# Kernel tuning notes

Hardware: AMD Instinct MI355X
Metric: run time of the kernel (lower is better)

Reference implementation:

```python
import jax, jax.numpy as jnp
import numpy as np

NUM_SPECIAL = 3  # rows 1..NUM_SPECIAL in special table; row 0 is padding (zeros)

def setup_inputs() -> dict:
    key = jax.random.key(0)
    ks = jax.random.split(key, 16)
    T, B, E, H, L, V = 128, 32, 512, 512, 2, 32000
    G = 4 * H
    s = 0.02
    special_emb = jax.random.normal(ks[1], (NUM_SPECIAL + 1, E), jnp.float32) * s
    special_emb = special_emb.at[0].set(0.0)  # padding_idx=0
    return {
        "ids": jax.random.randint(ks[0], (T, B), 0, V),
        "length_countdown": jax.random.uniform(ks[2], (T, B, 1), jnp.float32),
        "word_emb": jax.random.normal(ks[3], (V, E), jnp.float32) * s,
        "special_emb": special_emb,
        "h0": jax.random.normal(ks[4], (L, B, H), jnp.float32) * s,
        "c0": jax.random.normal(ks[5], (L, B, H), jnp.float32) * s,
        "prev_output": jnp.zeros((B, H), jnp.float32),
        "Wih0": jax.random.normal(ks[6], (G, E + H + 1), jnp.float32) * s,
        "Whh0": jax.random.normal(ks[7], (G, H), jnp.float32) * s,
        "bih0": jnp.zeros((G,), jnp.float32),
        "bhh0": jnp.zeros((G,), jnp.float32),
        "Wih1": jax.random.normal(ks[8], (G, H), jnp.float32) * s,
        "Whh1": jax.random.normal(ks[9], (G, H), jnp.float32) * s,
        "bih1": jnp.zeros((G,), jnp.float32),
        "bhh1": jnp.zeros((G,), jnp.float32),
        "Wg": jax.random.normal(ks[10], (V, H), jnp.float32) * s,
        "bg": jnp.zeros((V,), jnp.float32),
    }

def _lstm_cell(x, h, c, Wih, Whh, bih, bhh):
    gates = x @ Wih.T + bih + h @ Whh.T + bhh  # [B, 4H]
    i, f, g, o = jnp.split(gates, 4, axis=-1)  # torch LSTMCell gate order
    c_new = jax.nn.sigmoid(f) * c + jax.nn.sigmoid(i) * jnp.tanh(g)
    h_new = jax.nn.sigmoid(o) * jnp.tanh(c_new)
    return h_new, c_new

def reference(ids, length_countdown, word_emb, special_emb, h0, c0, prev_output,
              Wih0, Whh0, bih0, bhh0, Wih1, Whh1, bih1, bhh1, Wg, bg):
    # embeddings = word_embeddings(ids) + special_embeddings(special_ids(ids))
    sp_ids = jnp.where(ids < NUM_SPECIAL, ids + 1, 0)
    emb = word_emb[ids] + special_emb[sp_ids]                 # [T,B,E]
    rnn_in = jnp.concatenate([emb, length_countdown], axis=2)  # [T,B,E+1]

    Wihs = (Wih0, Wih1); Whhs = (Whh0, Whh1)
    bihs = (bih0, bih1); bhhs = (bhh0, bhh1)
    L = h0.shape[0]

    def step(carry, emb_t):
        out, h, c = carry
        x = jnp.concatenate([emb_t, out], axis=1)  # input feeding
        hs, cs = [], []
        for l in range(L):
            h_l, c_l = _lstm_cell(x, h[l], c[l], Wihs[l], Whhs[l], bihs[l], bhhs[l])
            x = h_l  # dropout=0
            hs.append(h_l); cs.append(c_l)
        out = x
        score = jax.nn.log_softmax(out @ Wg.T + bg, axis=-1)  # generator
        return (out, jnp.stack(hs), jnp.stack(cs)), score

    (out, hT, cT), scores = jax.lax.scan(step, (prev_output, h0, c0), rnn_in)
    return scores, (hT, cT), out
```

## Files before the change

kernel.cpp:

```cpp
#include <hip/hip_runtime.h>
#include <hip/hip_bf16.h>


typedef __attribute__((ext_vector_type(8))) short bf16x8;
typedef __attribute__((ext_vector_type(4))) float f32x4;
typedef __attribute__((ext_vector_type(2))) unsigned long long u64x2;

#define AS1 __attribute__((address_space(1)))
#define AS3 __attribute__((address_space(3)))
#define RLX __ATOMIC_RELAXED
#define AGT __HIP_MEMORY_SCOPE_AGENT

__device__ __forceinline__ unsigned short f2bf(float f) {
  unsigned int u = __builtin_bit_cast(unsigned int, f);
  u += 0x7fffu + ((u >> 16) & 1u);
  return (unsigned short)(u >> 16);
}

__device__ __forceinline__ void gl16(const void* g, void* l) {
  __builtin_amdgcn_global_load_lds((const AS1 unsigned int*)g,
                                   (AS3 unsigned int*)l, 16, 0, 0);
}

__device__ __forceinline__ float sigm(float x) { return 1.0f / (1.0f + __expf(-x)); }

__global__ __launch_bounds__(256, 1) void prep_k(
    const float* __restrict__ Wg,  const float* __restrict__ Wih0,
    const float* __restrict__ Whh0,const float* __restrict__ Wih1,
    const float* __restrict__ Whh1,const float* __restrict__ bih0,
    const float* __restrict__ bhh0,const float* __restrict__ bih1,
    const float* __restrict__ bhh1,const float* __restrict__ h0,
    const float* __restrict__ pout,
    unsigned short* __restrict__ WgBf, unsigned short* __restrict__ W0e,
    unsigned short* __restrict__ Wr0p, unsigned short* __restrict__ Wr1p,
    float* __restrict__ b1p, float* __restrict__ bias0c,
    float* __restrict__ wcd, unsigned short* __restrict__ H0X,
    unsigned short* __restrict__ FOUT, unsigned short* __restrict__ H1I)
{
  const long N0 = 16384000L;
  const long N1 = N0 + 1048576L;
  const long N2 = N1 + 2097152L;
  const long N3 = N2 + 2097152L;
  const long N4 = N3 + 2048L;
  const long N5 = N4 + 2048L;
  const long N6 = N5 + 2048L;
  const long N7 = N6 + 49152L;
  for (long i = blockIdx.x * 256L + threadIdx.x; i < N7; i += 256L * gridDim.x) {
    if (i < N0) {
      WgBf[i] = f2bf(Wg[i]);
    } else if (i < N1) {
      long k = i - N0; int g = (int)(k >> 9); int kk = (int)(k & 511);
      W0e[k] = f2bf(Wih0[g * 1025 + kk]);
    } else if (i < N2) {
      long k = i - N1; int gp = (int)(k >> 10); int kk = (int)(k & 1023);
      int j = gp >> 2, gate = gp & 3; int g = gate * 512 + j;
      float v = (kk < 512) ? Whh0[g * 512 + kk] : Wih0[g * 1025 + 513 + (kk - 512)];
      Wr0p[k] = f2bf(v);
    } else if (i < N3) {
      long k = i - N2; int gp = (int)(k >> 10); int kk = (int)(k & 1023);
      int j = gp >> 2, gate = gp & 3; int g = gate * 512 + j;
      float v = (kk < 512) ? Wih1[g * 512 + kk] : Whh1[g * 512 + (kk - 512)];
      Wr1p[k] = f2bf(v);
    } else if (i < N4) {
      int gp = (int)(i - N3); int j = gp >> 2, gate = gp & 3; int g = gate * 512 + j;
      b1p[gp] = bih1[g] + bhh1[g];
    } else if (i < N5) {
      int g = (int)(i - N4); bias0c[g] = bih0[g] + bhh0[g];
    } else if (i < N6) {
      int g = (int)(i - N5); wcd[g] = Wih0[g * 1025 + 512];
    } else {
      long k = i - N6;
      int sub = (int)(k >> 14);
      int e = (int)(k & 16383);
      int wgx = e >> 9, b = (e >> 4) & 31, jl = e & 15;
      int j = wgx * 16 + jl;
      float v = (sub == 0) ? h0[b * 512 + j]
              : (sub == 1) ? h0[16384 + b * 512 + j]
                           : pout[b * 512 + j];
      unsigned short* dst = (sub == 0) ? H0X : (sub == 1) ? H1I : FOUT;
      dst[e] = f2bf(v);
    }
  }
}

__global__ __launch_bounds__(256, 1) void emb_k(
    const int* __restrict__ ids, const float* __restrict__ wemb,
    const float* __restrict__ semb, unsigned short* __restrict__ ebf)
{
  const int tb = blockIdx.x;
  const int id = ids[tb];
  const int sp = (id < 3) ? (id + 1) : 0;
  const float* wr = wemb + (long)id * 512;
  const float* sr = semb + sp * 512;
  for (int i = threadIdx.x; i < 512; i += 256)
    ebf[tb * 512 + i] = f2bf(wr[i] + sr[i]);
}

template<int EPI>
__global__ __launch_bounds__(256, 1) void gemm_bt(
    const unsigned short* __restrict__ A,
    const unsigned short* __restrict__ B, int N,
    float* __restrict__ C,
    const float* __restrict__ e0, float* __restrict__ e1,
    const float* __restrict__ e2)
{
  __shared__ unsigned short sA[4096];
  __shared__ unsigned short sB[4096];
  __shared__ float pmw[128][2][2];
  const int tid = threadIdx.x;
  const int l = tid & 63, w = tid >> 6;
  const int nb = N >> 7;
  const int bid = blockIdx.x;
  const int bm = bid / nb, bn = bid - bm * nb;

  const int u0 = w * 128 + l;
  const int u1 = u0 + 64;
  const int r0 = u0 >> 2, c0 = (u0 & 3) ^ (r0 & 3);
  const int r1 = u1 >> 2, c1 = (u1 & 3) ^ (r1 & 3);
  const unsigned short* ga0 = A + (long)(bm * 128 + r0) * 512 + c0 * 8;
  const unsigned short* ga1 = A + (long)(bm * 128 + r1) * 512 + c1 * 8;
  const unsigned short* gb0 = B + (long)(bn * 128 + r0) * 512 + c0 * 8;
  const unsigned short* gb1 = B + (long)(bn * 128 + r1) * 512 + c1 * 8;
  unsigned short* la0 = sA + (w * 2 + 0) * 512;
  unsigned short* la1 = sA + (w * 2 + 1) * 512;
  unsigned short* lb0 = sB + (w * 2 + 0) * 512;
  unsigned short* lb1 = sB + (w * 2 + 1) * 512;

  const int fr = l & 15, fc = l >> 4;
  const int wm = w >> 1, wn = w & 1;
  int aoff[4], boff[4];
#pragma unroll
  for (int mi = 0; mi < 4; ++mi) {
    int row = wm * 64 + mi * 16 + fr;
    aoff[mi] = row * 64 + ((fc ^ (row & 3)) * 16);
  }
#pragma unroll
  for (int ni = 0; ni < 4; ++ni) {
    int row = wn * 64 + ni * 16 + fr;
    boff[ni] = row * 64 + ((fc ^ (row & 3)) * 16);
  }

  f32x4 acc[4][4];
#pragma unroll
  for (int i = 0; i < 4; ++i)
#pragma unroll
    for (int jq = 0; jq < 4; ++jq) acc[i][jq] = (f32x4){0.f, 0.f, 0.f, 0.f};

  for (int kt = 0; kt < 16; ++kt) {
    __syncthreads();
    gl16(ga0 + kt * 32, la0);
    gl16(ga1 + kt * 32, la1);
    gl16(gb0 + kt * 32, lb0);
    gl16(gb1 + kt * 32, lb1);
    asm volatile("s_waitcnt vmcnt(0)" ::: "memory");
    __syncthreads();
    bf16x8 av[4], bv[4];
#pragma unroll
    for (int mi = 0; mi < 4; ++mi)
      av[mi] = *(const bf16x8*)((const char*)sA + aoff[mi]);
#pragma unroll
    for (int ni = 0; ni < 4; ++ni)
      bv[ni] = *(const bf16x8*)((const char*)sB + boff[ni]);
#pragma unroll
    for (int mi = 0; mi < 4; ++mi)
#pragma unroll
      for (int ni = 0; ni < 4; ++ni)
        acc[mi][ni] = __builtin_amdgcn_mfma_f32_16x16x32_bf16(av[mi], bv[ni], acc[mi][ni], 0, 0, 0);
  }

  const int mbase = bm * 128 + wm * 64;
  const int nbase = bn * 128 + wn * 64;

  if (EPI == 0) {
#pragma unroll
    for (int mi = 0; mi < 4; ++mi)
#pragma unroll
      for (int ni = 0; ni < 4; ++ni) {
        const int col = nbase + ni * 16 + fr;
#pragma unroll
        for (int r = 0; r < 4; ++r) {
          const int row = mbase + mi * 16 + fc * 4 + r;
          const int gp = ((row & 511) << 2) | (row >> 9);
          float v = acc[mi][ni][r] + e0[row] + e2[col] * e1[row];
          C[(long)gp * N + col] = v;
        }
      }
  } else {
    float m2[4][4], s2[4][4];
#pragma unroll
    for (int mi = 0; mi < 4; ++mi)
#pragma unroll
      for (int r = 0; r < 4; ++r) { m2[mi][r] = -3.0e38f; s2[mi][r] = 0.f; }
#pragma unroll
    for (int mi = 0; mi < 4; ++mi)
#pragma unroll
      for (int ni = 0; ni < 4; ++ni) {
        const int col = nbase + ni * 16 + fr;
        const float bgc = e0[col];
#pragma unroll
        for (int r = 0; r < 4; ++r) {
          float v = acc[mi][ni][r] + bgc;
          acc[mi][ni][r] = v;
          C[(long)(mbase + mi * 16 + fc * 4 + r) * N + col] = v;
          m2[mi][r] = fmaxf(m2[mi][r], v);
        }
      }
#pragma unroll
    for (int mi = 0; mi < 4; ++mi)
#pragma unroll
      for (int r = 0; r < 4; ++r)
#pragma unroll
        for (int s = 1; s < 16; s <<= 1)
          m2[mi][r] = fmaxf(m2[mi][r], __shfl_xor(m2[mi][r], s));
#pragma unroll
    for (int mi = 0; mi < 4; ++mi)
#pragma unroll
      for (int ni = 0; ni < 4; ++ni)
#pragma unroll
        for (int r = 0; r < 4; ++r)
          s2[mi][r] += __expf(acc[mi][ni][r] - m2[mi][r]);
#pragma unroll
    for (int mi = 0; mi < 4; ++mi)
#pragma unroll
      for (int r = 0; r < 4; ++r)
#pragma unroll
        for (int s = 1; s < 16; s <<= 1)
          s2[mi][r] += __shfl_xor(s2[mi][r], s);
    if (fr == 0) {
#pragma unroll
      for (int mi = 0; mi < 4; ++mi)
#pragma unroll
        for (int r = 0; r < 4; ++r) {
          const int rl = wm * 64 + mi * 16 + fc * 4 + r;
          pmw[rl][wn][0] = m2[mi][r];
          pmw[rl][wn][1] = s2[mi][r];
        }
    }
    __syncthreads();
    if (tid < 128) {
      float ma = pmw[tid][0][0], sa = pmw[tid][0][1];
      float mb = pmw[tid][1][0], sb = pmw[tid][1][1];
      float M = fmaxf(ma, mb);
      float S = sa * __expf(ma - M) + sb * __expf(mb - M);
      float2* PMS = (float2*)e1;
      float2 o; o.x = M; o.y = S;
      PMS[(long)(bm * 128 + tid) * nb + bn] = o;
    }
  }
}

__global__ __launch_bounds__(256, 1) void lstm_seq(
    const unsigned short* __restrict__ Wr0p,
    const unsigned short* __restrict__ Wr1p,
    const float* __restrict__ P0t, const float* __restrict__ b1p,
    const float* __restrict__ c0in,
    unsigned short* __restrict__ H0X, unsigned short* __restrict__ H1X,
    const unsigned short* __restrict__ FOUT, const unsigned short* __restrict__ H1I,
    unsigned short* __restrict__ outbf, float* __restrict__ outs,
    unsigned int* __restrict__ flagA, unsigned int* __restrict__ flagB)
{
  const int tid = threadIdx.x;
  const int wg = blockIdx.x;
  const int l = tid & 63, w = tid >> 6;
  const int fr = l & 15, fc = l >> 4;

  __shared__ unsigned short sx[32768];
  __shared__ float sg[32][65];
  __shared__ unsigned short sh[32][16];

  const int b = tid & 31, jl0 = tid >> 5;
  const int sb = l >> 1, sjh = l & 1;

  float c0r[2], c1r[2], h0k[2], h1k[2];
#pragma unroll
  for (int jq = 0; jq < 2; ++jq) {
    c0r[jq] = c0in[b * 512 + wg * 16 + jl0 + jq * 8];
    c1r[jq] = c0in[16384 + b * 512 + wg * 16 + jl0 + jq * 8];
    h0k[jq] = 0.f; h1k[jq] = 0.f;
  }

  float b1v[8];
#pragma unroll
  for (int jq = 0; jq < 2; ++jq)
#pragma unroll
    for (int g = 0; g < 4; ++g)
      b1v[jq * 4 + g] = b1p[(wg * 16 + jl0 + jq * 8) * 4 + g];

  const char* sxb0 = (const char*)sx + fr * 2048;
  const char* sxb1 = (const char*)sx + (16 + fr) * 2048;
  const int xr = (fr & 7) << 4;
  const int wrow = (wg * 64 + w * 16 + fr) * 1024 + fc * 8;

  char* const sxw = (char*)sx + sb * 2048;
  const int sswz = (sb & 7) << 4;

#define STAGE2(srcp, half)                                                    \
  do {                                                                        \
    unsigned long long q0[8], q1[8];                                          \
    _Pragma("unroll")                                                         \
    for (int i = 0; i < 8; ++i) {                                             \
      int u = i * 256 + tid;                                                  \
      q0[i] = __hip_atomic_load((const unsigned long long*)(srcp) + u * 2,    \
                                RLX, AGT);                                    \
      q1[i] = __hip_atomic_load((const unsigned long long*)(srcp) + u * 2 + 1,\
                                RLX, AGT);                                    \
    }                                                                         \
    _Pragma("unroll")                                                         \
    for (int i = 0; i < 8; ++i) {                                             \
      int cb = (half) * 1024 + (i * 4 + w) * 32 + sjh * 16;                   \
      u64x2 v; v.x = q0[i]; v.y = q1[i];                                      \
      *(u64x2*)(sxw + (cb ^ sswz)) = v;                                       \
    }                                                                         \
  } while (0)

#define MFMA_HALF(Wp, k0, a0v, a1v)                                           \
  do {                                                                        \
    _Pragma("unroll")                                                         \
    for (int kt = (k0); kt < (k0) + 16; ++kt) {                               \
      bf16x8 bv = *(const bf16x8*)((Wp) + wrow + kt * 32);                    \
      bf16x8 x0 = *(const bf16x8*)(sxb0 + ((kt * 64 + fc * 16) ^ xr));        \
      bf16x8 x1 = *(const bf16x8*)(sxb1 + ((kt * 64 + fc * 16) ^ xr));        \
      a0v = __builtin_amdgcn_mfma_f32_16x16x32_bf16(x0, bv, a0v, 0, 0, 0);    \
      a1v = __builtin_amdgcn_mfma_f32_16x16x32_bf16(x1, bv, a1v, 0, 0, 0);    \
    }                                                                         \
  } while (0)

#define POLL(flags, tgt)                                                      \
  do {                                                                        \
    const unsigned int* fp = (flags) + ((l & 31) << 5);                       \
    for (;;) {                                                                \
      unsigned int f = __hip_atomic_load(fp, RLX, AGT);                       \
      if (__all((int)(f >= (unsigned int)(tgt)))) break;                      \
      __builtin_amdgcn_s_sleep(1);                                            \
    }                                                                         \
    asm volatile("" ::: "memory");                                            \
  } while (0)

  STAGE2(H0X, 0);
  __syncthreads();
  if (tid == 0)
    __hip_atomic_store(&flagB[wg << 5], 1u, RLX, AGT);

  for (int t = 0; t < 128; ++t) {
    float p0v[8];
#pragma unroll
    for (int jq = 0; jq < 2; ++jq)
#pragma unroll
      for (int g = 0; g < 4; ++g)
        p0v[jq * 4 + g] =
            P0t[(long)((wg * 16 + jl0 + jq * 8) * 4 + g) * 4096 + t * 32 + b];

    f32x4 accA0 = (f32x4){0.f, 0.f, 0.f, 0.f};
    f32x4 accA1 = (f32x4){0.f, 0.f, 0.f, 0.f};
    MFMA_HALF(Wr0p, 0, accA0, accA1);

    POLL(flagB, t + 1);
    if (t == 0) STAGE2(FOUT, 1); else STAGE2(H1X, 1);
    __syncthreads();
    MFMA_HALF(Wr0p, 16, accA0, accA1);
#pragma unroll
    for (int r = 0; r < 4; ++r) {
      sg[fc * 4 + r][w * 16 + fr] = accA0[r];
      sg[16 + fc * 4 + r][w * 16 + fr] = accA1[r];
    }
    __syncthreads();
#pragma unroll
    for (int jq = 0; jq < 2; ++jq) {
      const int jl = jl0 + jq * 8;
      float gi = sg[b][jl * 4 + 0] + p0v[jq * 4 + 0];
      float gf = sg[b][jl * 4 + 1] + p0v[jq * 4 + 1];
      float gg = sg[b][jl * 4 + 2] + p0v[jq * 4 + 2];
      float go = sg[b][jl * 4 + 3] + p0v[jq * 4 + 3];
      float cn = sigm(gf) * c0r[jq] + sigm(gi) * tanhf(gg);
      float hn = sigm(go) * tanhf(cn);
      c0r[jq] = cn; h0k[jq] = hn;
      sh[b][jl] = f2bf(hn);
    }
    __syncthreads();
    if (w == 0) {
      u64x2 v = *(const u64x2*)&sh[sb][sjh * 8];
      unsigned long long* dst =
          (unsigned long long*)(H0X + wg * 512 + sb * 16 + sjh * 8);
      __hip_atomic_store(dst,     v.x, RLX, AGT);
      __hip_atomic_store(dst + 1, v.y, RLX, AGT);
      asm volatile("s_waitcnt vmcnt(0)" ::: "memory");
      if (tid == 0)
        __hip_atomic_store(&flagA[wg << 5], (unsigned int)(t + 1), RLX, AGT);
    }

    f32x4 accB0 = (f32x4){0.f, 0.f, 0.f, 0.f};
    f32x4 accB1 = (f32x4){0.f, 0.f, 0.f, 0.f};
    if (t == 0) {
      STAGE2(H1I, 1);
      __syncthreads();
    }
    MFMA_HALF(Wr1p, 16, accB0, accB1);

    POLL(flagA, t + 1);
    STAGE2(H0X, 0);
    __syncthreads();
    MFMA_HALF(Wr1p, 0, accB0, accB1);
#pragma unroll
    for (int r = 0; r < 4; ++r) {
      sg[fc * 4 + r][w * 16 + fr] = accB0[r];
      sg[16 + fc * 4 + r][w * 16 + fr] = accB1[r];
    }
    __syncthreads();
#pragma unroll
    for (int jq = 0; jq < 2; ++jq) {
      const int jl = jl0 + jq * 8;
      float gi = sg[b][jl * 4 + 0] + b1v[jq * 4 + 0];
      float gf = sg[b][jl * 4 + 1] + b1v[jq * 4 + 1];
      float gg = sg[b][jl * 4 + 2] + b1v[jq * 4 + 2];
      float go = sg[b][jl * 4 + 3] + b1v[jq * 4 + 3];
      float cn = sigm(gf) * c1r[jq] + sigm(gi) * tanhf(gg);
      float hn = sigm(go) * tanhf(cn);
      c1r[jq] = cn; h1k[jq] = hn;
      sh[b][jl] = f2bf(hn);
    }
    __syncthreads();
    if (w == 0) {
      u64x2 v = *(const u64x2*)&sh[sb][sjh * 8];
      unsigned long long* dst =
          (unsigned long long*)(H1X + wg * 512 + sb * 16 + sjh * 8);
      __hip_atomic_store(dst,     v.x, RLX, AGT);
      __hip_atomic_store(dst + 1, v.y, RLX, AGT);
      asm volatile("s_waitcnt vmcnt(0)" ::: "memory");
      if (tid == 0)
        __hip_atomic_store(&flagB[wg << 5], (unsigned int)(t + 2), RLX, AGT);
    } else if (w == 1) {
      u64x2 v = *(const u64x2*)&sh[sb][sjh * 8];
      *(u64x2*)(outbf + (t * 32 + sb) * 512 + wg * 16 + sjh * 8) = v;
    }
  }
#undef STAGE2
#undef MFMA_HALF
#undef POLL

  float* hT = outs + 131072000;
  float* cT = outs + 131072000 + 32768;
  float* oT = outs + 131072000 + 65536;
#pragma unroll
  for (int jq = 0; jq < 2; ++jq) {
    const int j = wg * 16 + jl0 + jq * 8;
    hT[b * 512 + j] = h0k[jq];
    hT[16384 + b * 512 + j] = h1k[jq];
    cT[b * 512 + j] = c0r[jq];
    cT[16384 + b * 512 + j] = c1r[jq];
    oT[b * 512 + j] = h1k[jq];
  }
}

__global__ __launch_bounds__(256, 1) void lse_fix(float* __restrict__ sc,
                                                  const float2* __restrict__ pms)
{
  const long row = blockIdx.x;
  float4* p4 = (float4*)(sc + row * 32000L);
  const int tid = threadIdx.x;
  float m = -3.0e38f, s = 0.0f;
  if (tid < 250) {
    float2 p = pms[row * 250 + tid];
    m = p.x; s = p.y;
  }
#pragma unroll
  for (int off = 32; off > 0; off >>= 1) {
    float mo = __shfl_down(m, off);
    float so = __shfl_down(s, off);
    float mn = fmaxf(m, mo);
    s = s * __expf(m - mn) + so * __expf(mo - mn);
    m = mn;
  }
  __shared__ float lm[4], ls[4], lse_sh;
  if ((tid & 63) == 0) { lm[tid >> 6] = m; ls[tid >> 6] = s; }
  __syncthreads();
  if (tid == 0) {
    float M = lm[0], S = ls[0];
#pragma unroll
    for (int i = 1; i < 4; ++i) {
      float mn = fmaxf(M, lm[i]);
      S = S * __expf(M - mn) + ls[i] * __expf(lm[i] - mn);
      M = mn;
    }
    lse_sh = M + __logf(S);
  }
  __syncthreads();
  const float lse = lse_sh;
  for (int i = tid; i < 8000; i += 256) {
    float4 v = p4[i];
    v.x -= lse; v.y -= lse; v.z -= lse; v.w -= lse;
    p4[i] = v;
  }
}

extern "C" void kernel_launch(void* const* d_in, const int* in_sizes, int n_in,
                              void* d_out, int out_size, void* d_ws, size_t ws_size,
                              hipStream_t stream) {
  const int*   ids  = (const int*)d_in[0];
  const float* cd   = (const float*)d_in[1];
  const float* wemb = (const float*)d_in[2];
  const float* semb = (const float*)d_in[3];
  const float* h0   = (const float*)d_in[4];
  const float* c0   = (const float*)d_in[5];
  const float* pout = (const float*)d_in[6];
  const float* Wih0 = (const float*)d_in[7];
  const float* Whh0 = (const float*)d_in[8];
  const float* bih0 = (const float*)d_in[9];
  const float* bhh0 = (const float*)d_in[10];
  const float* Wih1 = (const float*)d_in[11];
  const float* Whh1 = (const float*)d_in[12];
  const float* bih1 = (const float*)d_in[13];
  const float* bhh1 = (const float*)d_in[14];
  const float* Wg   = (const float*)d_in[15];
  const float* bg   = (const float*)d_in[16];
  float* out = (float*)d_out;

  char* ws = (char*)d_ws;
  unsigned short* WgBf   = (unsigned short*)(ws);
  unsigned short* W0e    = (unsigned short*)(ws + 32768000);
  unsigned short* Wr0p   = (unsigned short*)(ws + 34865152);
  unsigned short* Wr1p   = (unsigned short*)(ws + 39059456);
  float*          b1p    = (float*)(ws + 43253760);
  float*          bias0c = (float*)(ws + 43261952);
  float*          wcd    = (float*)(ws + 43270144);
  unsigned short* embbf  = (unsigned short*)(ws + 43278336);
  unsigned short* outbf  = (unsigned short*)(ws + 47472640);
  float*          P0t    = (float*)(ws + 51666944);
  float*          PMS    = (float*)(ws + 51666944);
  unsigned int*   flagA  = (unsigned int*)(ws + 85221376);
  unsigned int*   flagB  = (unsigned int*)(ws + 85225472);
  unsigned short* H0X    = (unsigned short*)(ws + 85229568);
  unsigned short* H1X    = (unsigned short*)(ws + 85262336);
  unsigned short* FOUT   = (unsigned short*)(ws + 85295104);
  unsigned short* H1I    = (unsigned short*)(ws + 85327872);

  hipMemsetAsync((void*)flagA, 0, 8192, stream);

  prep_k<<<8192, 256, 0, stream>>>(Wg, Wih0, Whh0, Wih1, Whh1,
                                   bih0, bhh0, bih1, bhh1, h0, pout,
                                   WgBf, W0e, Wr0p, Wr1p, b1p, bias0c, wcd,
                                   H0X, FOUT, H1I);

  emb_k<<<4096, 256, 0, stream>>>(ids, wemb, semb, embbf);

  gemm_bt<0><<<512, 256, 0, stream>>>(W0e, embbf, 4096, P0t, bias0c, wcd, cd);

  lstm_seq<<<32, 256, 0, stream>>>(Wr0p, Wr1p, P0t, b1p, c0,
                                   H0X, H1X, FOUT, H1I, outbf, out, flagA, flagB);

  gemm_bt<1><<<8000, 256, 0, stream>>>(outbf, WgBf, 32000, out, bg, PMS, nullptr);

  lse_fix<<<4096, 256, 0, stream>>>(out, (const float2*)PMS);
}
```

Before: 1.911 ms.

## Overlap generator GEMM with LSTM recurrence via persistent consumer blocks and flags

Merges the vocabulary-projection GEMM into the LSTM kernel launch. 224 extra blocks persistently process 128x128 output tiles and poll per-timestep flags that the 32 recurrent blocks publish after writing each h1 row block, so the generator runs alongside the sequential recurrence instead of after it. Partial max/sum results are written into the P0t buffer region. This relies on all 256 blocks being co-resident, since the recurrent blocks spin-wait on each other. It also adds atomic loads and polling overhead, and the generator blocks may compete with the latency-critical recurrent blocks for memory bandwidth.

```diff
diff --git a/kernel.cpp b/kernel.cpp
--- a/kernel.cpp
+++ b/kernel.cpp
@@ -10,6 +10,7 @@
 #define AS3 __attribute__((address_space(3)))
 #define RLX __ATOMIC_RELAXED
 #define AGT __HIP_MEMORY_SCOPE_AGENT
+#define NGEN 224
 
 __device__ __forceinline__ unsigned short f2bf(float f) {
   unsigned int u = __builtin_bit_cast(unsigned int, f);
@@ -96,17 +97,15 @@
     ebf[tb * 512 + i] = f2bf(wr[i] + sr[i]);
 }
 
-template<int EPI>
-__global__ __launch_bounds__(256, 1) void gemm_bt(
+__global__ __launch_bounds__(256, 1) void gemm_p0(
     const unsigned short* __restrict__ A,
     const unsigned short* __restrict__ B, int N,
     float* __restrict__ C,
-    const float* __restrict__ e0, float* __restrict__ e1,
+    const float* __restrict__ e0, const float* __restrict__ e1,
     const float* __restrict__ e2)
 {
   __shared__ unsigned short sA[4096];
   __shared__ unsigned short sB[4096];
-  __shared__ float pmw[128][2][2];
   const int tid = threadIdx.x;
   const int l = tid & 63, w = tid >> 6;
   const int nb = N >> 7;
@@ -170,129 +169,69 @@
 
   const int mbase = bm * 128 + wm * 64;
   const int nbase = bn * 128 + wn * 64;
-
-  if (EPI == 0) {
-#pragma unroll
-    for (int mi = 0; mi < 4; ++mi)
-#pragma unroll
-      for (int ni = 0; ni < 4; ++ni) {
-        const int col = nbase + ni * 16 + fr;
-#pragma unroll
-        for (int r = 0; r < 4; ++r) {
-          const int row = mbase + mi * 16 + fc * 4 + r;
-          const int gp = ((row & 511) << 2) | (row >> 9);
-          float v = acc[mi][ni][r] + e0[row] + e2[col] * e1[row];
-          C[(long)gp * N + col] = v;
-        }
-      }
-  } else {
-    float m2[4][4], s2[4][4];
-#pragma unroll
-    for (int mi = 0; mi < 4; ++mi)
-#pragma unroll
-      for (int r = 0; r < 4; ++r) { m2[mi][r] = -3.0e38f; s2[mi][r] = 0.f; }
-#pragma unroll
-    for (int mi = 0; mi < 4; ++mi)
-#pragma unroll
-      for (int ni = 0; ni < 4; ++ni) {
-        const int col = nbase + ni * 16 + fr;
-        const float bgc = e0[col];
-#pragma unroll
-        for (int r = 0; r < 4; ++r) {
-          float v = acc[mi][ni][r] + bgc;
-          acc[mi][ni][r] = v;
-          C[(long)(mbase + mi * 16 + fc * 4 + r) * N + col] = v;
-          m2[mi][r] = fmaxf(m2[mi][r], v);
-        }
-      }
-#pragma unroll
-    for (int mi = 0; mi < 4; ++mi)
-#pragma unroll
-      for (int r = 0; r < 4; ++r)
-#pragma unroll
-        for (int s = 1; s < 16; s <<= 1)
-          m2[mi][r] = fmaxf(m2[mi][r], __shfl_xor(m2[mi][r], s));
-#pragma unroll
-    for (int mi = 0; mi < 4; ++mi)
-#pragma unroll
-      for (int ni = 0; ni < 4; ++ni)
-#pragma unroll
-        for (int r = 0; r < 4; ++r)
-          s2[mi][r] += __expf(acc[mi][ni][r] - m2[mi][r]);
-#pragma unroll
-    for (int mi = 0; mi < 4; ++mi)
-#pragma unroll
-      for (int r = 0; r < 4; ++r)
-#pragma unroll
-        for (int s = 1; s < 16; s <<= 1)
-          s2[mi][r] += __shfl_xor(s2[mi][r], s);
-    if (fr == 0) {
-#pragma unroll
-      for (int mi = 0; mi < 4; ++mi)
-#pragma unroll
-        for (int r = 0; r < 4; ++r) {
-          const int rl = wm * 64 + mi * 16 + fc * 4 + r;
-          pmw[rl][wn][0] = m2[mi][r];
-          pmw[rl][wn][1] = s2[mi][r];
-        }
-    }
-    __syncthreads();
-    if (tid < 128) {
-      float ma = pmw[tid][0][0], sa = pmw[tid][0][1];
-      float mb = pmw[tid][1][0], sb = pmw[tid][1][1];
-      float M = fmaxf(ma, mb);
-      float S = sa * __expf(ma - M) + sb * __expf(mb - M);
-      float2* PMS = (float2*)e1;
-      float2 o; o.x = M; o.y = S;
-      PMS[(long)(bm * 128 + tid) * nb + bn] = o;
-    }
-  }
+#pragma unroll
+  for (int mi = 0; mi < 4; ++mi)
+#pragma unroll
+    for (int ni = 0; ni < 4; ++ni) {
+      const int col = nbase + ni * 16 + fr;
+#pragma unroll
+      for (int r = 0; r < 4; ++r) {
+        const int row = mbase + mi * 16 + fc * 4 + r;
+        const int gp = ((row & 511) << 2) | (row >> 9);
+        float v = acc[mi][ni][r] + e0[row] + e2[col] * e1[row];
+        C[(long)gp * N + col] = v;
+      }
+    }
 }
 
 __global__ __launch_bounds__(256, 1) void lstm_seq(
     const unsigned short* __restrict__ Wr0p,
     const unsigned short* __restrict__ Wr1p,
-    const float* __restrict__ P0t, const float* __restrict__ b1p,
+    float* __restrict__ P0t, const float* __restrict__ b1p,
     const float* __restrict__ c0in,
     unsigned short* __restrict__ H0X, unsigned short* __restrict__ H1X,
     const unsigned short* __restrict__ FOUT, const unsigned short* __restrict__ H1I,
     unsigned short* __restrict__ outbf, float* __restrict__ outs,
-    unsigned int* __restrict__ flagA, unsigned int* __restrict__ flagB)
+    unsigned int* __restrict__ flagA, unsigned int* __restrict__ flagB,
+    unsigned int* __restrict__ flagC,
+    const unsigned short* __restrict__ WgBf, const float* __restrict__ bg)
 {
   const int tid = threadIdx.x;
-  const int wg = blockIdx.x;
-  const int l = tid & 63, w = tid >> 6;
-  const int fr = l & 15, fc = l >> 4;
-
-  __shared__ unsigned short sx[32768];
-  __shared__ float sg[32][65];
-  __shared__ unsigned short sh[32][16];
-
-  const int b = tid & 31, jl0 = tid >> 5;
-  const int sb = l >> 1, sjh = l & 1;
-
-  float c0r[2], c1r[2], h0k[2], h1k[2];
-#pragma unroll
-  for (int jq = 0; jq < 2; ++jq) {
-    c0r[jq] = c0in[b * 512 + wg * 16 + jl0 + jq * 8];
-    c1r[jq] = c0in[16384 + b * 512 + wg * 16 + jl0 + jq * 8];
-    h0k[jq] = 0.f; h1k[jq] = 0.f;
-  }
-
-  float b1v[8];
-#pragma unroll
-  for (int jq = 0; jq < 2; ++jq)
-#pragma unroll
-    for (int g = 0; g < 4; ++g)
-      b1v[jq * 4 + g] = b1p[(wg * 16 + jl0 + jq * 8) * 4 + g];
-
-  const char* sxb0 = (const char*)sx + fr * 2048;
-  const char* sxb1 = (const char*)sx + (16 + fr) * 2048;
-  const int xr = (fr & 7) << 4;
-  const int wrow = (wg * 64 + w * 16 + fr) * 1024 + fc * 8;
-
-  char* const sxw = (char*)sx + sb * 2048;
-  const int sswz = (sb & 7) << 4;
+  __shared__ char smem[75264] __attribute__((aligned(16)));
+
+  if (blockIdx.x < 32) {
+    unsigned short* sx = (unsigned short*)smem;
+    float (*sg)[65] = (float(*)[65])(smem + 65536);
+    unsigned short (*sh)[16] = (unsigned short(*)[16])(smem + 73856);
+
+    const int wg = blockIdx.x;
+    const int l = tid & 63, w = tid >> 6;
+    const int fr = l & 15, fc = l >> 4;
+    const int b = tid & 31, jl0 = tid >> 5;
+    const int sb = l >> 1, sjh = l & 1;
+
+    float c0r[2], c1r[2], h0k[2], h1k[2];
+#pragma unroll
+    for (int jq = 0; jq < 2; ++jq) {
+      c0r[jq] = c0in[b * 512 + wg * 16 + jl0 + jq * 8];
+      c1r[jq] = c0in[16384 + b * 512 + wg * 16 + jl0 + jq * 8];
+      h0k[jq] = 0.f; h1k[jq] = 0.f;
+    }
+
+    float b1v[8];
+#pragma unroll
+    for (int jq = 0; jq < 2; ++jq)
+#pragma unroll
+      for (int g = 0; g < 4; ++g)
+        b1v[jq * 4 + g] = b1p[(wg * 16 + jl0 + jq * 8) * 4 + g];
+
+    const char* sxb0 = (const char*)sx + fr * 2048;
+    const char* sxb1 = (const char*)sx + (16 + fr) * 2048;
+    const int xr = (fr & 7) << 4;
+    const int wrow = (wg * 64 + w * 16 + fr) * 1024 + fc * 8;
+
+    char* const sxw = (char*)sx + sb * 2048;
+    const int sswz = (sb & 7) << 4;
 
 #define STAGE2(srcp, half)                                                    \
   do {                                                                        \
@@ -336,131 +275,287 @@
     asm volatile("" ::: "memory");                                            \
   } while (0)
 
-  STAGE2(H0X, 0);
-  __syncthreads();
-  if (tid == 0)
-    __hip_atomic_store(&flagB[wg << 5], 1u, RLX, AGT);
-
-  for (int t = 0; t < 128; ++t) {
-    float p0v[8];
-#pragma unroll
-    for (int jq = 0; jq < 2; ++jq)
-#pragma unroll
-      for (int g = 0; g < 4; ++g)
-        p0v[jq * 4 + g] =
-            P0t[(long)((wg * 16 + jl0 + jq * 8) * 4 + g) * 4096 + t * 32 + b];
-
-    f32x4 accA0 = (f32x4){0.f, 0.f, 0.f, 0.f};
-    f32x4 accA1 = (f32x4){0.f, 0.f, 0.f, 0.f};
-    MFMA_HALF(Wr0p, 0, accA0, accA1);
-
-    POLL(flagB, t + 1);
-    if (t == 0) STAGE2(FOUT, 1); else STAGE2(H1X, 1);
-    __syncthreads();
-    MFMA_HALF(Wr0p, 16, accA0, accA1);
-#pragma unroll
-    for (int r = 0; r < 4; ++r) {
-      sg[fc * 4 + r][w * 16 + fr] = accA0[r];
-      sg[16 + fc * 4 + r][w * 16 + fr] = accA1[r];
-    }
-    __syncthreads();
-#pragma unroll
-    for (int jq = 0; jq < 2; ++jq) {
-      const int jl = jl0 + jq * 8;
-      float gi = sg[b][jl * 4 + 0] + p0v[jq * 4 + 0];
-      float gf = sg[b][jl * 4 + 1] + p0v[jq * 4 + 1];
-      float gg = sg[b][jl * 4 + 2] + p0v[jq * 4 + 2];
-      float go = sg[b][jl * 4 + 3] + p0v[jq * 4 + 3];
-      float cn = sigm(gf) * c0r[jq] + sigm(gi) * tanhf(gg);
-      float hn = sigm(go) * tanhf(cn);
-      c0r[jq] = cn; h0k[jq] = hn;
-      sh[b][jl] = f2bf(hn);
-    }
-    __syncthreads();
-    if (w == 0) {
-      u64x2 v = *(const u64x2*)&sh[sb][sjh * 8];
-      unsigned long long* dst =
-          (unsigned long long*)(H0X + wg * 512 + sb * 16 + sjh * 8);
-      __hip_atomic_store(dst,     v.x, RLX, AGT);
-      __hip_atomic_store(dst + 1, v.y, RLX, AGT);
-      asm volatile("s_waitcnt vmcnt(0)" ::: "memory");
-      if (tid == 0)
-        __hip_atomic_store(&flagA[wg << 5], (unsigned int)(t + 1), RLX, AGT);
-    }
-
-    f32x4 accB0 = (f32x4){0.f, 0.f, 0.f, 0.f};
-    f32x4 accB1 = (f32x4){0.f, 0.f, 0.f, 0.f};
-    if (t == 0) {
-      STAGE2(H1I, 1);
-      __syncthreads();
-    }
-    MFMA_HALF(Wr1p, 16, accB0, accB1);
-
-    POLL(flagA, t + 1);
     STAGE2(H0X, 0);
     __syncthreads();
-    MFMA_HALF(Wr1p, 0, accB0, accB1);
-#pragma unroll
-    for (int r = 0; r < 4; ++r) {
-      sg[fc * 4 + r][w * 16 + fr] = accB0[r];
-      sg[16 + fc * 4 + r][w * 16 + fr] = accB1[r];
-    }
-    __syncthreads();
-#pragma unroll
-    for (int jq = 0; jq < 2; ++jq) {
-      const int jl = jl0 + jq * 8;
-      float gi = sg[b][jl * 4 + 0] + b1v[jq * 4 + 0];
-      float gf = sg[b][jl * 4 + 1] + b1v[jq * 4 + 1];
-      float gg = sg[b][jl * 4 + 2] + b1v[jq * 4 + 2];
-      float go = sg[b][jl * 4 + 3] + b1v[jq * 4 + 3];
-      float cn = sigm(gf) * c1r[jq] + sigm(gi) * tanhf(gg);
-      float hn = sigm(go) * tanhf(cn);
-      c1r[jq] = cn; h1k[jq] = hn;
-      sh[b][jl] = f2bf(hn);
-    }
-    __syncthreads();
-    if (w == 0) {
-      u64x2 v = *(const u64x2*)&sh[sb][sjh * 8];
-      unsigned long long* dst =
-          (unsigned long long*)(H1X + wg * 512 + sb * 16 + sjh * 8);
-      __hip_atomic_store(dst,     v.x, RLX, AGT);
-      __hip_atomic_store(dst + 1, v.y, RLX, AGT);
-      asm volatile("s_waitcnt vmcnt(0)" ::: "memory");
-      if (tid == 0)
-        __hip_atomic_store(&flagB[wg << 5], (unsigned int)(t + 2), RLX, AGT);
-    } else if (w == 1) {
-      u64x2 v = *(const u64x2*)&sh[sb][sjh * 8];
-      *(u64x2*)(outbf + (t * 32 + sb) * 512 + wg * 16 + sjh * 8) = v;
-    }
-  }
+    if (tid == 0)
+      __hip_atomic_store(&flagB[wg << 5], 1u, RLX, AGT);
+
+    for (int t = 0; t < 128; ++t) {
+      float p0v[8];
+#pragma unroll
+      for (int jq = 0; jq < 2; ++jq)
+#pragma unroll
+        for (int g = 0; g < 4; ++g)
+          p0v[jq * 4 + g] =
+              P0t[(long)((wg * 16 + jl0 + jq * 8) * 4 + g) * 4096 + t * 32 + b];
+
+      f32x4 accA0 = (f32x4){0.f, 0.f, 0.f, 0.f};
+      f32x4 accA1 = (f32x4){0.f, 0.f, 0.f, 0.f};
+      MFMA_HALF(Wr0p, 0, accA0, accA1);
+
+      POLL(flagB, t + 1);
+      if (t == 0) STAGE2(FOUT, 1); else STAGE2(H1X, 1);
+      __syncthreads();
+      MFMA_HALF(Wr0p, 16, accA0, accA1);
+#pragma unroll
+      for (int r = 0; r < 4; ++r) {
+        sg[fc * 4 + r][w * 16 + fr] = accA0[r];
+        sg[16 + fc * 4 + r][w * 16 + fr] = accA1[r];
+      }
+      __syncthreads();
+#pragma unroll
+      for (int jq = 0; jq < 2; ++jq) {
+        const int jl = jl0 + jq * 8;
+        float gi = sg[b][jl * 4 + 0] + p0v[jq * 4 + 0];
+        float gf = sg[b][jl * 4 + 1] + p0v[jq * 4 + 1];
+        float gg = sg[b][jl * 4 + 2] + p0v[jq * 4 + 2];
+        float go = sg[b][jl * 4 + 3] + p0v[jq * 4 + 3];
+        float cn = sigm(gf) * c0r[jq] + sigm(gi) * tanhf(gg);
+        float hn = sigm(go) * tanhf(cn);
+        c0r[jq] = cn; h0k[jq] = hn;
+        sh[b][jl] = f2bf(hn);
+      }
+      __syncthreads();
+      if (w == 0) {
+        u64x2 v = *(const u64x2*)&sh[sb][sjh * 8];
+        unsigned long long* dst =
+            (unsigned long long*)(H0X + wg * 512 + sb * 16 + sjh * 8);
+        __hip_atomic_store(dst,     v.x, RLX, AGT);
+        __hip_atomic_store(dst + 1, v.y, RLX, AGT);
+        asm volatile("s_waitcnt vmcnt(0)" ::: "memory");
+        if (tid == 0)
+          __hip_atomic_store(&flagA[wg << 5], (unsigned int)(t + 1), RLX, AGT);
+      }
+
+      f32x4 accB0 = (f32x4){0.f, 0.f, 0.f, 0.f};
+      f32x4 accB1 = (f32x4){0.f, 0.f, 0.f, 0.f};
+      if (t == 0) {
+        STAGE2(H1I, 1);
+        __syncthreads();
+      }
+      MFMA_HALF(Wr1p, 16, accB0, accB1);
+
+      POLL(flagA, t + 1);
+      STAGE2(H0X, 0);
+      __syncthreads();
+      MFMA_HALF(Wr1p, 0, accB0, accB1);
+#pragma unroll
+      for (int r = 0; r < 4; ++r) {
+        sg[fc * 4 + r][w * 16 + fr] = accB0[r];
+        sg[16 + fc * 4 + r][w * 16 + fr] = accB1[r];
+      }
+      __syncthreads();
+#pragma unroll
+      for (int jq = 0; jq < 2; ++jq) {
+        const int jl = jl0 + jq * 8;
+        float gi = sg[b][jl * 4 + 0] + b1v[jq * 4 + 0];
+        float gf = sg[b][jl * 4 + 1] + b1v[jq * 4 + 1];
+        float gg = sg[b][jl * 4 + 2] + b1v[jq * 4 + 2];
+        float go = sg[b][jl * 4 + 3] + b1v[jq * 4 + 3];
+        float cn = sigm(gf) * c1r[jq] + sigm(gi) * tanhf(gg);
+        float hn = sigm(go) * tanhf(cn);
+        c1r[jq] = cn; h1k[jq] = hn;
+        sh[b][jl] = f2bf(hn);
+      }
+      __syncthreads();
+      if (w == 0) {
+        u64x2 v = *(const u64x2*)&sh[sb][sjh * 8];
+        unsigned long long* dst =
+            (unsigned long long*)(H1X + wg * 512 + sb * 16 + sjh * 8);
+        __hip_atomic_store(dst,     v.x, RLX, AGT);
+        __hip_atomic_store(dst + 1, v.y, RLX, AGT);
+        asm volatile("s_waitcnt vmcnt(0)" ::: "memory");
+        if (tid == 0)
+          __hip_atomic_store(&flagB[wg << 5], (unsigned int)(t + 2), RLX, AGT);
+      } else if (w == 1) {
+        const unsigned long long* s = (const unsigned long long*)&sh[sb][sjh * 8];
+        unsigned long long* dst =
+            (unsigned long long*)(outbf + (t * 32 + sb) * 512 + wg * 16 + sjh * 8);
+        __hip_atomic_store(dst,     s[0], RLX, AGT);
+        __hip_atomic_store(dst + 1, s[1], RLX, AGT);
+        asm volatile("s_waitcnt vmcnt(0)" ::: "memory");
+        if (l == 0)
+          __hip_atomic_store(&flagC[wg << 5], (unsigned int)(t + 1), RLX, AGT);
+      }
+    }
 #undef STAGE2
 #undef MFMA_HALF
 #undef POLL
 
-  float* hT = outs + 131072000;
-  float* cT = outs + 131072000 + 32768;
-  float* oT = outs + 131072000 + 65536;
-#pragma unroll
-  for (int jq = 0; jq < 2; ++jq) {
-    const int j = wg * 16 + jl0 + jq * 8;
-    hT[b * 512 + j] = h0k[jq];
-    hT[16384 + b * 512 + j] = h1k[jq];
-    cT[b * 512 + j] = c0r[jq];
-    cT[16384 + b * 512 + j] = c1r[jq];
-    oT[b * 512 + j] = h1k[jq];
+    float* hT = outs + 131072000;
+    float* cT = outs + 131072000 + 32768;
+    float* oT = outs + 131072000 + 65536;
+#pragma unroll
+    for (int jq = 0; jq < 2; ++jq) {
+      const int j = wg * 16 + jl0 + jq * 8;
+      hT[b * 512 + j] = h0k[jq];
+      hT[16384 + b * 512 + j] = h1k[jq];
+      cT[b * 512 + j] = c0r[jq];
+      cT[16384 + b * 512 + j] = c1r[jq];
+      oT[b * 512 + j] = h1k[jq];
+    }
+    return;
+  }
+
+  {
+    unsigned short* sA = (unsigned short*)smem;
+    unsigned short* sB = (unsigned short*)(smem + 8192);
+    float (*pmw)[2][2] = (float(*)[2][2])(smem + 16384);
+
+    const int g = (int)blockIdx.x - 32;
+    const int l = tid & 63, w = tid >> 6;
+    const int fr = l & 15, fc = l >> 4;
+    const int wm = w >> 1, wn = w & 1;
+
+    const int u0 = w * 128 + l, u1 = u0 + 64;
+    const int r0 = u0 >> 2, c0 = (u0 & 3) ^ (r0 & 3);
+    const int r1 = u1 >> 2, c1 = (u1 & 3) ^ (r1 & 3);
+    unsigned short* lb0 = sB + (w * 2 + 0) * 512;
+    unsigned short* lb1 = sB + (w * 2 + 1) * 512;
+
+    int aoff[4], boff[4];
+#pragma unroll
+    for (int mi = 0; mi < 4; ++mi) {
+      int row = wm * 64 + mi * 16 + fr;
+      aoff[mi] = row * 64 + ((fc ^ (row & 3)) * 16);
+    }
+#pragma unroll
+    for (int ni = 0; ni < 4; ++ni) {
+      int row = wn * 64 + ni * 16 + fr;
+      boff[ni] = row * 64 + ((fc ^ (row & 3)) * 16);
+    }
+
+    for (int job = g; job < 8000; job += NGEN) {
+      const int bm = job / 250, bn = job - bm * 250;
+
+      if (w == 0) {
+        const unsigned int* fp = flagC + ((l & 31) << 5);
+        const unsigned int tgt = (unsigned int)(4 * bm + 4);
+        for (;;) {
+          unsigned int f = __hip_atomic_load(fp, RLX, AGT);
+          if (__all((int)(f >= tgt))) break;
+          __builtin_amdgcn_s_sleep(16);
+        }
+        asm volatile("" ::: "memory");
+      }
+      __syncthreads();
+
+      const unsigned short* Ab0 = outbf + (long)(bm * 128 + r0) * 512 + c0 * 8;
+      const unsigned short* Ab1 = outbf + (long)(bm * 128 + r1) * 512 + c1 * 8;
+      const unsigned short* gb0 = WgBf + (long)(bn * 128 + r0) * 512 + c0 * 8;
+      const unsigned short* gb1 = WgBf + (long)(bn * 128 + r1) * 512 + c1 * 8;
+
+      f32x4 acc[4][4];
+#pragma unroll
+      for (int i = 0; i < 4; ++i)
+#pragma unroll
+        for (int jq = 0; jq < 4; ++jq) acc[i][jq] = (f32x4){0.f, 0.f, 0.f, 0.f};
+
+      for (int kt = 0; kt < 16; ++kt) {
+        __syncthreads();
+        unsigned long long a0x = __hip_atomic_load((const unsigned long long*)(Ab0 + kt * 32),     RLX, AGT);
+        unsigned long long a0y = __hip_atomic_load((const unsigned long long*)(Ab0 + kt * 32) + 1, RLX, AGT);
+        unsigned long long a1x = __hip_atomic_load((const unsigned long long*)(Ab1 + kt * 32),     RLX, AGT);
+        unsigned long long a1y = __hip_atomic_load((const unsigned long long*)(Ab1 + kt * 32) + 1, RLX, AGT);
+        gl16(gb0 + kt * 32, lb0);
+        gl16(gb1 + kt * 32, lb1);
+        { u64x2 va; va.x = a0x; va.y = a0y; *(u64x2*)((char*)sA + u0 * 16) = va; }
+        { u64x2 va; va.x = a1x; va.y = a1y; *(u64x2*)((char*)sA + u1 * 16) = va; }
+        asm volatile("s_waitcnt vmcnt(0)" ::: "memory");
+        __syncthreads();
+        bf16x8 av[4], bv[4];
+#pragma unroll
+        for (int mi = 0; mi < 4; ++mi)
+          av[mi] = *(const bf16x8*)((const char*)sA + aoff[mi]);
+#pragma unroll
+        for (int ni = 0; ni < 4; ++ni)
+          bv[ni] = *(const bf16x8*)((const char*)sB + boff[ni]);
+#pragma unroll
+        for (int mi = 0; mi < 4; ++mi)
+#pragma unroll
+          for (int ni = 0; ni < 4; ++ni)
+            acc[mi][ni] = __builtin_amdgcn_mfma_f32_16x16x32_bf16(av[mi], bv[ni], acc[mi][ni], 0, 0, 0);
+      }
+
+      const int mbase = bm * 128 + wm * 64;
+      const int nbase = bn * 128 + wn * 64;
+      float m2[4][4], s2[4][4];
+#pragma unroll
+      for (int mi = 0; mi < 4; ++mi)
+#pragma unroll
+        for (int r = 0; r < 4; ++r) { m2[mi][r] = -3.0e38f; s2[mi][r] = 0.f; }
+#pragma unroll
+      for (int mi = 0; mi < 4; ++mi)
+#pragma unroll
+        for (int ni = 0; ni < 4; ++ni) {
+          const int col = nbase + ni * 16 + fr;
+          const float bgc = bg[col];
+#pragma unroll
+          for (int r = 0; r < 4; ++r) {
+            float v = acc[mi][ni][r] + bgc;
+            acc[mi][ni][r] = v;
+            outs[(long)(mbase + mi * 16 + fc * 4 + r) * 32000L + col] = v;
+            m2[mi][r] = fmaxf(m2[mi][r], v);
+          }
+        }
+#pragma unroll
+      for (int mi = 0; mi < 4; ++mi)
+#pragma unroll
+        for (int r = 0; r < 4; ++r)
+#pragma unroll
+          for (int s = 1; s < 16; s <<= 1)
+            m2[mi][r] = fmaxf(m2[mi][r], __shfl_xor(m2[mi][r], s));
+#pragma unroll
+      for (int mi = 0; mi < 4; ++mi)
+#pragma unroll
+        for (int ni = 0; ni < 4; ++ni)
+#pragma unroll
+          for (int r = 0; r < 4; ++r)
+            s2[mi][r] += __expf(acc[mi][ni][r] - m2[mi][r]);
+#pragma unroll
+      for (int mi = 0; mi < 4; ++mi)
+#pragma unroll
+        for (int r = 0; r < 4; ++r)
+#pragma unroll
+          for (int s = 1; s < 16; s <<= 1)
+            s2[mi][r] += __shfl_xor(s2[mi][r], s);
+      if (fr == 0) {
+#pragma unroll
+        for (int mi = 0; mi < 4; ++mi)
+#pragma unroll
+          for (int r = 0; r < 4; ++r) {
+            const int rl = wm * 64 + mi * 16 + fc * 4 + r;
+            pmw[rl][wn][0] = m2[mi][r];
+            pmw[rl][wn][1] = s2[mi][r];
+          }
+      }
+      __syncthreads();
+      if (tid < 128) {
+        float ma = pmw[tid][0][0], sa = pmw[tid][0][1];
+        float mb = pmw[tid][1][0], sb2 = pmw[tid][1][1];
+        float M = fmaxf(ma, mb);
+        float S = sa * __expf(ma - M) + sb2 * __expf(mb - M);
+        int q2 = 2 * (tid * 250 + bn);
+        float* p = P0t + ((long)(q2 >> 7)) * 4096 + 128L * bm + (q2 & 127);
+        p[0] = M; p[1] = S;
+      }
+      __syncthreads();
+    }
   }
 }
 
 __global__ __launch_bounds__(256, 1) void lse_fix(float* __restrict__ sc,
-                                                  const float2* __restrict__ pms)
+                                                  const float* __restrict__ pmsbase)
 {
   const long row = blockIdx.x;
+  const int bm = (int)(row >> 7), rl = (int)(row & 127);
   float4* p4 = (float4*)(sc + row * 32000L);
   const int tid = threadIdx.x;
   float m = -3.0e38f, s = 0.0f;
   if (tid < 250) {
-    float2 p = pms[row * 250 + tid];
-    m = p.x; s = p.y;
+    int q2 = 2 * (rl * 250 + tid);
+    const float* p = pmsbase + ((long)(q2 >> 7)) * 4096 + 128L * bm + (q2 & 127);
+    m = p[0]; s = p[1];
   }
 #pragma unroll
   for (int off = 32; off > 0; off >>= 1) {
@@ -525,15 +620,16 @@
   unsigned short* embbf  = (unsigned short*)(ws + 43278336);
   unsigned short* outbf  = (unsigned short*)(ws + 47472640);
   float*          P0t    = (float*)(ws + 51666944);
-  float*          PMS    = (float*)(ws + 51666944);
   unsigned int*   flagA  = (unsigned int*)(ws + 85221376);
   unsigned int*   flagB  = (unsigned int*)(ws + 85225472);
   unsigned short* H0X    = (unsigned short*)(ws + 85229568);
   unsigned short* H1X    = (unsigned short*)(ws + 85262336);
   unsigned short* FOUT   = (unsigned short*)(ws + 85295104);
   unsigned short* H1I    = (unsigned short*)(ws + 85327872);
+  unsigned int*   flagC  = (unsigned int*)(ws + 85360640);
 
   hipMemsetAsync((void*)flagA, 0, 8192, stream);
+  hipMemsetAsync((void*)flagC, 0, 4096, stream);
 
   prep_k<<<8192, 256, 0, stream>>>(Wg, Wih0, Whh0, Wih1, Whh1,
                                    bih0, bhh0, bih1, bhh1, h0, pout,
@@ -542,12 +638,11 @@
 
   emb_k<<<4096, 256, 0, stream>>>(ids, wemb, semb, embbf);
 
-  gemm_bt<0><<<512, 256, 0, stream>>>(W0e, embbf, 4096, P0t, bias0c, wcd, cd);
-
-  lstm_seq<<<32, 256, 0, stream>>>(Wr0p, Wr1p, P0t, b1p, c0,
-                                   H0X, H1X, FOUT, H1I, outbf, out, flagA, flagB);
-
-  gemm_bt<1><<<8000, 256, 0, stream>>>(outbf, WgBf, 32000, out, bg, PMS, nullptr);
-
-  lse_fix<<<4096, 256, 0, stream>>>(out, (const float2*)PMS);
-}
+  gemm_p0<<<512, 256, 0, stream>>>(W0e, embbf, 4096, P0t, bias0c, wcd, cd);
+
+  lstm_seq<<<32 + NGEN, 256, 0, stream>>>(Wr0p, Wr1p, P0t, b1p, c0,
+                                          H0X, H1X, FOUT, H1I, outbf, out,
+                                          flagA, flagB, flagC, WgBf, bg);
+
+  lse_fix<<<4096, 256, 0, stream>>>(out, P0t);
+}
```

New measurement: 1.797 ms. 1.06x faster.
